# Kernel tuning notes

Measured on AMD Instinct MI355X. Metric: run time of the kernel, lower is better.

The kernel has to match this reference:

```python
import jax, jax.numpy as jnp
import numpy as np

N, C, T, V, K = 32, 256, 64, 25, 3   # batch, in_channels, frames, joints, adjacency partitions
D = 256                               # out_channels
KT = 9                                # temporal kernel size
PAD = (KT - 1) // 2
EPS = 1e-5                            # BatchNorm eps (torch default)


def setup_inputs() -> dict:
    key = jax.random.key(0)
    ks = jax.random.split(key, 5)
    x = jax.random.normal(ks[0], (N, C, T, V), jnp.float32)
    A = jax.random.uniform(ks[1], (K, V, V), jnp.float32)           # learnable adjacency
    W_gcn = jax.random.normal(ks[2], (K, D, C), jnp.float32) * (2.0 / C) ** 0.5  # K stacked 1x1 convs
    b_gcn = jnp.zeros((K, D), jnp.float32)
    W_tcn = jax.random.normal(ks[3], (D, D, KT, 1), jnp.float32) * (2.0 / (D * KT)) ** 0.5  # kaiming fan_out
    b_tcn = jnp.zeros((D,), jnp.float32)
    gamma = jnp.ones((D,), jnp.float32)   # bn_init(bn, 1)
    beta = jnp.zeros((D,), jnp.float32)
    return dict(x=x, A=A, W_gcn=W_gcn, b_gcn=b_gcn, W_tcn=W_tcn,
                b_tcn=b_tcn, gamma=gamma, beta=beta)


def reference(x, A, W_gcn, b_gcn, W_tcn, b_tcn, gamma, beta):
    # ---- GCN: per-partition 1x1 conv over channels, then graph aggregation via A[k], summed over k ----
    # y[k,n,d,t,v] = sum_c W_gcn[k,d,c] * x[n,c,t,v] + b_gcn[k,d]
    y = jnp.einsum('kdc,nctv->kndtv', W_gcn, x) + b_gcn[:, None, :, None, None]
    # aggregate neighbors: sum_v y[k,n,d,t,v] * A[k,v,w], accumulated over partitions k
    y = jnp.einsum('kndtv,kvw->ndtw', y, A)        # [N, D, T, V]

    # ---- TCN: (9,1) temporal conv + BatchNorm2d (batch statistics) ----
    z = jax.lax.conv_general_dilated(
        y, W_tcn, window_strides=(1, 1), padding=((PAD, PAD), (0, 0)),
        dimension_numbers=('NCHW', 'OIHW', 'NCHW'))
    z = z + b_tcn[None, :, None, None]
    mean = jnp.mean(z, axis=(0, 2, 3), keepdims=True)
    var = jnp.mean((z - mean) ** 2, axis=(0, 2, 3), keepdims=True)  # biased, as torch BN training fwd
    z = gamma[None, :, None, None] * (z - mean) * jax.lax.rsqrt(var + EPS) + beta[None, :, None, None]

    # ---- residual (identity branch: in==out, stride==1) + ReLU ----
    return jax.nn.relu(z + x)
```

## Files before the change

### kernel.cpp

```cpp
#include <hip/hip_runtime.h>
#include <math.h>

typedef unsigned short u16;
typedef short v8s __attribute__((ext_vector_type(8)));
typedef float v4f __attribute__((ext_vector_type(4)));

#define AS1 __attribute__((address_space(1)))
#define AS3 __attribute__((address_space(3)))

__device__ __forceinline__ float bf2f(u16 u) {
    union { unsigned int i; float f; } c; c.i = ((unsigned int)u) << 16; return c.f;
}
__device__ __forceinline__ u16 f2bf(float f) {
    union { float f; unsigned int i; } c; c.f = f;
    unsigned int u = c.i;
    return (u16)((u + 0x7FFFu + ((u >> 16) & 1u)) >> 16);
}
__device__ __forceinline__ void gload_lds16(const void* g, void* l) {
    __builtin_amdgcn_global_load_lds((const AS1 void*)(uintptr_t)g,
                                     (AS3 void*)(unsigned int)(uintptr_t)l,
                                     16, 0, 0);
}

#define Nn 32
#define Tt 64
#define Vv 25
#define NP 51200
#define NBLK 200

__global__ __launch_bounds__(256) void prep_kernel(
    const float* __restrict__ Wg, const float* __restrict__ Wt,
    const float* __restrict__ A, const float* __restrict__ bg,
    u16* __restrict__ Wgb, u16* __restrict__ Wtb,
    float* __restrict__ bias2, float* __restrict__ zpad)
{
    const int idx = blockIdx.x * 256 + threadIdx.x;
    const int stride = gridDim.x * 256;
    for (int i = idx; i < 256 * 2304; i += stride) {
        int d = i / 2304, r = i - d * 2304, dt = r >> 8, c = r & 255;
        Wtb[i] = f2bf(Wt[(d * 256 + c) * 9 + dt]);
    }
    for (int i = idx; i < 256 * 768; i += stride) {
        int d = i / 768, r = i - d * 768, k = r >> 8, c = r & 255;
        Wgb[i] = f2bf(Wg[(k * 256 + d) * 256 + c]);
    }
    for (int i = idx; i < 25 * 256; i += stride) {
        int w = i >> 8, d = i & 255;
        float s = 0.f;
        for (int k = 0; k < 3; ++k) {
            float cs = 0.f;
            for (int v = 0; v < 25; ++v) cs += A[(k * 25 + v) * 25 + w];
            s += bg[k * 256 + d] * cs;
        }
        bias2[i] = s;
    }
    for (int i = idx; i < 256; i += stride) zpad[i] = 0.f;
}

__global__ __launch_bounds__(256) void xa_kernel(
    const float* __restrict__ x, const float* __restrict__ A,
    u16* __restrict__ xa2)
{
    const int t = blockIdx.x, n = blockIdx.y;
    const int tid = threadIdx.x;
    __shared__ float xs[256 * 25];

    for (int i = tid; i < 6400; i += 256) {
        int c = i / 25, v = i - c * 25;
        xs[i] = x[((n * 256 + c) * 64 + t) * 25 + v];
    }
    __syncthreads();

    float xr[25];
    #pragma unroll
    for (int v = 0; v < 25; ++v) xr[v] = xs[tid * 25 + v];

    const size_t pbase = ((size_t)n * 64 + t) * 25;
    #pragma unroll 1
    for (int k = 0; k < 3; ++k) {
        float o[25];
        #pragma unroll
        for (int w = 0; w < 25; ++w) {
            float acc = 0.f;
            #pragma unroll
            for (int v = 0; v < 25; ++v)
                acc = fmaf(xr[v], A[(k * 25 + v) * 25 + w], acc);
            o[w] = acc;
        }
        u16* dst = xa2 + k * 256 + tid;
        #pragma unroll
        for (int w = 0; w < 25; ++w)
            dst[(pbase + w) * 768] = f2bf(o[w]);
    }
}

template<int KTOT, bool TCN>
__global__ __launch_bounds__(512) void gemm_kernel(
    const u16* __restrict__ Ad, const u16* __restrict__ Bw,
    const float* __restrict__ bias, u16* __restrict__ outB,
    float* __restrict__ psum, float* __restrict__ psq,
    const u16* __restrict__ zpad)
{
    constexpr int NT = KTOT / 64;
    __shared__ u16 smem[32768];

    const int tid = threadIdx.x;
    const int wid = tid >> 6, lane = tid & 63;
    const int lr = lane & 15, hk = lane >> 4;
    const int wm = wid >> 2, wn = wid & 3;
    const int rA = lane >> 3, sA = lane & 7;

    const int orig = blockIdx.x;
    const int m = (orig & 7) * 25 + (orig >> 3);

    u16* As = smem;
    u16* Bs = smem + 16384;

    v4f acc[8][4];
    const v4f vzero = {0.f, 0.f, 0.f, 0.f};
    #pragma unroll
    for (int mf = 0; mf < 8; ++mf)
        #pragma unroll
        for (int nf = 0; nf < 4; ++nf) acc[mf][nf] = vzero;

    for (int kt = 0; kt < NT; ++kt) {
        #pragma unroll
        for (int i = 0; i < 4; ++i) {
            const int ch = wid + i * 8;
            const int row = ch * 8 + rA;
            const int ss = sA ^ rA;
            const u16* srcA;
            if (TCN) {
                const int dt = kt >> 2, c0 = (kt & 3) << 6;
                const int p = m * 256 + row;
                const int t = (p % 1600) / 25;
                const int tp = t + dt - 4;
                srcA = ((unsigned)tp < 64u)
                     ? (Ad + (size_t)(p + (dt - 4) * 25) * 256 + c0 + ss * 8)
                     : zpad;
            } else {
                srcA = Ad + (size_t)(m * 256 + row) * 768 + kt * 64 + ss * 8;
            }
            gload_lds16(srcA, (char*)As + ch * 1024);
            gload_lds16(Bw + (size_t)row * KTOT + kt * 64 + ss * 8,
                        (char*)Bs + ch * 1024);
        }
        __syncthreads();

        #pragma unroll
        for (int kk = 0; kk < 2; ++kk) {
            v8s a[8], b[4];
            #pragma unroll
            for (int mf = 0; mf < 8; ++mf) {
                const int row = wm * 128 + mf * 16 + lr;
                const int slot = kk * 4 + hk;
                a[mf] = *(const v8s*)((const char*)As + row * 128 + ((slot ^ (row & 7)) << 4));
            }
            #pragma unroll
            for (int nf = 0; nf < 4; ++nf) {
                const int row = wn * 64 + nf * 16 + lr;
                const int slot = kk * 4 + hk;
                b[nf] = *(const v8s*)((const char*)Bs + row * 128 + ((slot ^ (row & 7)) << 4));
            }
            #pragma unroll
            for (int mf = 0; mf < 8; ++mf)
                #pragma unroll
                for (int nf = 0; nf < 4; ++nf)
                    acc[mf][nf] = __builtin_amdgcn_mfma_f32_16x16x32_bf16(
                        a[mf], b[nf], acc[mf][nf], 0, 0, 0);
        }
        __syncthreads();
    }

    if (!TCN) {
        #pragma unroll
        for (int mf = 0; mf < 8; ++mf) {
            #pragma unroll
            for (int j = 0; j < 4; ++j) {
                const int p = m * 256 + wm * 128 + mf * 16 + hk * 4 + j;
                const int w = p % 25;
                #pragma unroll
                for (int nf = 0; nf < 4; ++nf) {
                    const int d = wn * 64 + nf * 16 + lr;
                    outB[(size_t)p * 256 + d] = f2bf(acc[mf][nf][j] + bias[w * 256 + d]);
                }
            }
        }
    } else {
        float s[4], q[4];
        #pragma unroll
        for (int nf = 0; nf < 4; ++nf) {
            const int d = wn * 64 + nf * 16 + lr;
            const float bb = bias[d];
            s[nf] = 0.f; q[nf] = 0.f;
            #pragma unroll
            for (int mf = 0; mf < 8; ++mf) {
                #pragma unroll
                for (int j = 0; j < 4; ++j) {
                    const int p = m * 256 + wm * 128 + mf * 16 + hk * 4 + j;
                    const float zz = acc[mf][nf][j] + bb;
                    outB[(size_t)p * 256 + d] = f2bf(zz);
                    s[nf] += zz; q[nf] += zz * zz;
                }
            }
            s[nf] += __shfl_xor(s[nf], 16); s[nf] += __shfl_xor(s[nf], 32);
            q[nf] += __shfl_xor(q[nf], 16); q[nf] += __shfl_xor(q[nf], 32);
        }
        __syncthreads();
        float* red = (float*)smem;
        if (hk == 0) {
            #pragma unroll
            for (int nf = 0; nf < 4; ++nf) {
                const int d = wn * 64 + nf * 16 + lr;
                red[wm * 256 + d] = s[nf];
                red[512 + wm * 256 + d] = q[nf];
            }
        }
        __syncthreads();
        if (tid < 256) {
            psum[(size_t)tid * NBLK + m] = red[tid] + red[256 + tid];
            psq[(size_t)tid * NBLK + m]  = red[512 + tid] + red[768 + tid];
        }
    }
}

__global__ __launch_bounds__(256) void bn_stats_kernel(
    const float* __restrict__ psum, const float* __restrict__ psq,
    const float* __restrict__ gamma, const float* __restrict__ beta,
    float* __restrict__ scale, float* __restrict__ shift)
{
    const int d = blockIdx.x, tid = threadIdx.x;
    float s = 0.f, q = 0.f;
    for (int i = tid; i < NBLK; i += 256) {
        s += psum[(size_t)d * NBLK + i];
        q += psq[(size_t)d * NBLK + i];
    }
    #pragma unroll
    for (int off = 32; off; off >>= 1) {
        s += __shfl_down(s, off);
        q += __shfl_down(q, off);
    }
    __shared__ float rs[4], rq[4];
    if ((tid & 63) == 0) { rs[tid >> 6] = s; rq[tid >> 6] = q; }
    __syncthreads();
    if (tid == 0) {
        s = rs[0] + rs[1] + rs[2] + rs[3];
        q = rq[0] + rq[1] + rq[2] + rq[3];
        const float mean = s / 51200.f;
        const float var = q / 51200.f - mean * mean;
        const float inv = rsqrtf(var + 1e-5f);
        scale[d] = gamma[d] * inv;
        shift[d] = beta[d] - gamma[d] * inv * mean;
    }
}

__global__ __launch_bounds__(256) void bn_apply_kernel(
    const u16* __restrict__ zb, const float* __restrict__ x,
    const float* __restrict__ scale, const float* __restrict__ shift,
    float* __restrict__ out)
{
    const int chunk = blockIdx.x;
    const int n = blockIdx.y;
    const int tid = threadIdx.x;
    __shared__ u16 zs[128 * 66];
    const size_t p0 = (size_t)n * 1600 + chunk * 64;

    for (int half = 0; half < 2; ++half) {
        const int d0 = half * 128;
        if (half) __syncthreads();
        for (int i = tid; i < 128 * 64; i += 256) {
            const int pl = i >> 7, dl = i & 127;
            zs[dl * 66 + pl] = zb[(p0 + pl) * 256 + d0 + dl];
        }
        __syncthreads();
        for (int i = tid; i < 128 * 64; i += 256) {
            const int dl = i >> 6, j = i & 63;
            const int d = d0 + dl;
            const size_t addr = ((size_t)n * 256 + d) * 1600 + chunk * 64 + j;
            const float r = bf2f(zs[dl * 66 + j]) * scale[d] + shift[d] + x[addr];
            out[addr] = fmaxf(r, 0.f);
        }
    }
}

extern "C" void kernel_launch(void* const* d_in, const int* in_sizes, int n_in,
                              void* d_out, int out_size, void* d_ws, size_t ws_size,
                              hipStream_t stream)
{
    const float* x     = (const float*)d_in[0];
    const float* A     = (const float*)d_in[1];
    const float* Wg    = (const float*)d_in[2];
    const float* bg    = (const float*)d_in[3];
    const float* Wt    = (const float*)d_in[4];
    const float* bt    = (const float*)d_in[5];
    const float* gamma = (const float*)d_in[6];
    const float* beta  = (const float*)d_in[7];
    float* out = (float*)d_out;

    char* w = (char*)d_ws;
    u16*   xa2   = (u16*)(w);
    u16*   y2T   = (u16*)(w + 78643200);
    u16*   zb    = (u16*)(w + 104857600);
    u16*   Wgb   = (u16*)(w + 131072000);
    u16*   Wtb   = (u16*)(w + 131465216);
    float* bias2 = (float*)(w + 132644864);
    float* psum  = (float*)(w + 132670464);
    float* psq   = (float*)(w + 133080064);
    float* scale = (float*)(w + 133489664);
    float* shift = (float*)(w + 133490688);
    float* zpad  = (float*)(w + 133491712);

    prep_kernel<<<128, 256, 0, stream>>>(Wg, Wt, A, bg, Wgb, Wtb, bias2, zpad);
    xa_kernel<<<dim3(64, 32), 256, 0, stream>>>(x, A, xa2);
    gemm_kernel<768, false><<<NBLK, 512, 0, stream>>>(xa2, Wgb, bias2, y2T,
                                                      nullptr, nullptr, (const u16*)zpad);
    gemm_kernel<2304, true><<<NBLK, 512, 0, stream>>>(y2T, Wtb, bt, zb,
                                                      psum, psq, (const u16*)zpad);
    bn_stats_kernel<<<256, 256, 0, stream>>>(psum, psq, gamma, beta, scale, shift);
    bn_apply_kernel<<<dim3(25, 32), 256, 0, stream>>>(zb, x, scale, shift, out);
}
```

Before: 196.8 us.

## Double-buffer LDS tiles with async prefetch two stages ahead in GEMM

Splits the shared-memory tile into two buffers and issues global-to-LDS loads for tile kt+2 while the MFMAs run on the current tile. Explicit vmcnt waits and barriers replace the per-iteration __syncthreads pair. A and B fragments for both k-halves are loaded into registers before the barrier so the buffer can be refilled early, and MFMA priority is raised with s_setprio. The aim is to hide global load latency behind compute, at the cost of twice the LDS (128KB per block), more registers, and a launch_bounds hint of 2 blocks per CU that the LDS size may not allow.

```diff
diff --git a/kernel.cpp b/kernel.cpp
--- a/kernel.cpp
+++ b/kernel.cpp
@@ -95,14 +95,14 @@
 }
 
 template<int KTOT, bool TCN>
-__global__ __launch_bounds__(512) void gemm_kernel(
+__global__ __launch_bounds__(512, 2) void gemm_kernel(
     const u16* __restrict__ Ad, const u16* __restrict__ Bw,
     const float* __restrict__ bias, u16* __restrict__ outB,
     float* __restrict__ psum, float* __restrict__ psq,
     const u16* __restrict__ zpad)
 {
     constexpr int NT = KTOT / 64;
-    __shared__ u16 smem[32768];
+    __shared__ u16 smem[2][32768];
 
     const int tid = threadIdx.x;
     const int wid = tid >> 6, lane = tid & 63;
@@ -113,9 +113,6 @@
     const int orig = blockIdx.x;
     const int m = (orig & 7) * 25 + (orig >> 3);
 
-    u16* As = smem;
-    u16* Bs = smem + 16384;
-
     v4f acc[8][4];
     const v4f vzero = {0.f, 0.f, 0.f, 0.f};
     #pragma unroll
@@ -123,54 +120,103 @@
         #pragma unroll
         for (int nf = 0; nf < 4; ++nf) acc[mf][nf] = vzero;
 
+#define STAGE(buf, ktv)                                                        \
+    {                                                                          \
+        _Pragma("unroll")                                                      \
+        for (int i = 0; i < 4; ++i) {                                          \
+            const int ch = wid + i * 8;                             \
+            const int row = ch * 8 + rA;                           \
+            const int ss = sA ^ rA;                           \
+            const u16* srcA;                                                   \
+            if (TCN) {                                                         \
+                const int dt = (ktv) >> 2, c0 = ((ktv)&3) << 6;                \
+                const int p = m * 256 + row;                                   \
+                const int t = (p % 1600) / 25;                                 \
+                const int tp = t + dt - 4;                                     \
+                srcA = ((unsigned)tp < 64u)                                    \
+                     ? (Ad + (size_t)(p + (dt - 4) * 25) * 256 + c0 + ss * 8)  \
+                     : zpad;                                                   \
+            } else {                                                           \
+                srcA = Ad + (size_t)(m * 256 + row) * 768 + (ktv)*64 + ss * 8; \
+            }                                                                  \
+            gload_lds16(srcA, (char*)&smem[buf][0] + ch * 1024);               \
+            gload_lds16(Bw + (size_t)row * KTOT + (ktv)*64 + ss * 8,           \
+                        (char*)&smem[buf][0] + 32768 + ch * 1024);             \
+        }                                                                      \
+    }
+
+#define LDA_(dst, As_, mfv, kkv)                                               \
+    {                                                                          \
+        const int row = wm * 128 + (mfv)*16 + lr;                              \
+        dst = *(const v8s*)((const char*)(As_) + row * 128 +                   \
+                            ((((kkv)*4 + hk) ^ (row & 7)) << 4));              \
+    }
+#define LDB_(dst, Bs_, nfv, kkv)                                               \
+    {                                                                          \
+        const int row = wn * 64 + (nfv)*16 + lr;                               \
+        dst = *(const v8s*)((const char*)(Bs_) + row * 128 +                   \
+                            ((((kkv)*4 + hk) ^ (row & 7)) << 4));              \
+    }
+
+    STAGE(0, 0);
+    if (NT > 1) STAGE(1, 1);
+    if (NT > 1) asm volatile("s_waitcnt vmcnt(8)" ::: "memory");
+    else        asm volatile("s_waitcnt vmcnt(0)" ::: "memory");
+    __builtin_amdgcn_sched_barrier(0);
+    __builtin_amdgcn_s_barrier();
+
+    #pragma unroll 1
     for (int kt = 0; kt < NT; ++kt) {
-        #pragma unroll
-        for (int i = 0; i < 4; ++i) {
-            const int ch = wid + i * 8;
-            const int row = ch * 8 + rA;
-            const int ss = sA ^ rA;
-            const u16* srcA;
-            if (TCN) {
-                const int dt = kt >> 2, c0 = (kt & 3) << 6;
-                const int p = m * 256 + row;
-                const int t = (p % 1600) / 25;
-                const int tp = t + dt - 4;
-                srcA = ((unsigned)tp < 64u)
-                     ? (Ad + (size_t)(p + (dt - 4) * 25) * 256 + c0 + ss * 8)
-                     : zpad;
-            } else {
-                srcA = Ad + (size_t)(m * 256 + row) * 768 + kt * 64 + ss * 8;
-            }
-            gload_lds16(srcA, (char*)As + ch * 1024);
-            gload_lds16(Bw + (size_t)row * KTOT + kt * 64 + ss * 8,
-                        (char*)Bs + ch * 1024);
-        }
-        __syncthreads();
-
-        #pragma unroll
-        for (int kk = 0; kk < 2; ++kk) {
-            v8s a[8], b[4];
-            #pragma unroll
-            for (int mf = 0; mf < 8; ++mf) {
-                const int row = wm * 128 + mf * 16 + lr;
-                const int slot = kk * 4 + hk;
-                a[mf] = *(const v8s*)((const char*)As + row * 128 + ((slot ^ (row & 7)) << 4));
-            }
-            #pragma unroll
-            for (int nf = 0; nf < 4; ++nf) {
-                const int row = wn * 64 + nf * 16 + lr;
-                const int slot = kk * 4 + hk;
-                b[nf] = *(const v8s*)((const char*)Bs + row * 128 + ((slot ^ (row & 7)) << 4));
-            }
-            #pragma unroll
-            for (int mf = 0; mf < 8; ++mf)
-                #pragma unroll
-                for (int nf = 0; nf < 4; ++nf)
-                    acc[mf][nf] = __builtin_amdgcn_mfma_f32_16x16x32_bf16(
-                        a[mf], b[nf], acc[mf][nf], 0, 0, 0);
-        }
-        __syncthreads();
-    }
+        const int cur = kt & 1;
+        const u16* As = &smem[cur][0];
+        const u16* Bs = As + 16384;
+
+        v8s a0[8], a1[8], b0[4], b1[4];
+        #pragma unroll
+        for (int nf = 0; nf < 4; ++nf) LDB_(b0[nf], Bs, nf, 0);
+        #pragma unroll
+        for (int mf = 0; mf < 8; ++mf) LDA_(a0[mf], As, mf, 0);
+        #pragma unroll
+        for (int nf = 0; nf < 4; ++nf) LDB_(b1[nf], Bs, nf, 1);
+        #pragma unroll
+        for (int mf = 0; mf < 8; ++mf) LDA_(a1[mf], As, mf, 1);
+        asm volatile("s_waitcnt lgkmcnt(0)" ::: "memory");
+        __builtin_amdgcn_sched_barrier(0);
+        __builtin_amdgcn_s_barrier();
+        __builtin_amdgcn_sched_barrier(0);
+
+        if (kt + 2 < NT) STAGE(cur, kt + 2);
+        __builtin_amdgcn_sched_barrier(0);
+
+        __builtin_amdgcn_s_setprio(1);
+        #pragma unroll
+        for (int mf = 0; mf < 8; ++mf)
+            #pragma unroll
+            for (int nf = 0; nf < 4; ++nf)
+                acc[mf][nf] = __builtin_amdgcn_mfma_f32_16x16x32_bf16(
+                    a0[mf], b0[nf], acc[mf][nf], 0, 0, 0);
+        #pragma unroll
+        for (int mf = 0; mf < 8; ++mf)
+            #pragma unroll
+            for (int nf = 0; nf < 4; ++nf)
+                acc[mf][nf] = __builtin_amdgcn_mfma_f32_16x16x32_bf16(
+                    a1[mf], b1[nf], acc[mf][nf], 0, 0, 0);
+        __builtin_amdgcn_s_setprio(0);
+        __builtin_amdgcn_sched_barrier(0);
+
+        if (kt + 2 < NT) {
+            asm volatile("s_waitcnt vmcnt(8)" ::: "memory");
+            __builtin_amdgcn_sched_barrier(0);
+            __builtin_amdgcn_s_barrier();
+        } else if (kt + 1 < NT) {
+            asm volatile("s_waitcnt vmcnt(0)" ::: "memory");
+            __builtin_amdgcn_sched_barrier(0);
+            __builtin_amdgcn_s_barrier();
+        }
+    }
+#undef STAGE
+#undef LDA_
+#undef LDB_
 
     if (!TCN) {
         #pragma unroll
@@ -207,7 +253,7 @@
             q[nf] += __shfl_xor(q[nf], 16); q[nf] += __shfl_xor(q[nf], 32);
         }
         __syncthreads();
-        float* red = (float*)smem;
+        float* red = (float*)&smem[0][0];
         if (hk == 0) {
             #pragma unroll
             for (int nf = 0; nf < 4; ++nf) {
```

After: 186.3 us. 1.06x faster.

## Pre-pack weights into MFMA fragment order and halve GEMM M-tile

Applied to the files above, without the earlier changes.

The prep kernel now writes both weight matrices in the exact per-lane MFMA fragment order. Each wave then loads its B operands straight from global memory into registers, so B no longer goes through LDS. The M tile per block shrinks from 256 to 128 rows and the grid grows from 200 to 400 blocks, which fills more CUs and cuts LDS and register use. The trade-off is that B fragments are re-read from cache by every block and wave with no LDS sharing, and each block now does less reuse per load.

```diff
diff --git a/kernel.cpp b/kernel.cpp
--- a/kernel.cpp
+++ b/kernel.cpp
@@ -26,23 +26,31 @@
 #define Tt 64
 #define Vv 25
 #define NP 51200
-#define NBLK 200
+#define NBLK 400
 
 __global__ __launch_bounds__(256) void prep_kernel(
     const float* __restrict__ Wg, const float* __restrict__ Wt,
     const float* __restrict__ A, const float* __restrict__ bg,
-    u16* __restrict__ Wgb, u16* __restrict__ Wtb,
+    u16* __restrict__ Bpg, u16* __restrict__ Bpt,
     float* __restrict__ bias2, float* __restrict__ zpad)
 {
     const int idx = blockIdx.x * 256 + threadIdx.x;
     const int stride = gridDim.x * 256;
-    for (int i = idx; i < 256 * 2304; i += stride) {
-        int d = i / 2304, r = i - d * 2304, dt = r >> 8, c = r & 255;
-        Wtb[i] = f2bf(Wt[(d * 256 + c) * 9 + dt]);
-    }
-    for (int i = idx; i < 256 * 768; i += stride) {
-        int d = i / 768, r = i - d * 768, k = r >> 8, c = r & 255;
-        Wgb[i] = f2bf(Wg[(k * 256 + d) * 256 + c]);
+    for (int i = idx; i < 589824; i += stride) {
+        const int e = i & 7, lane = (i >> 3) & 63, rest = i >> 9;
+        const int kk = rest & 1, nf = (rest >> 1) & 3, wn = (rest >> 3) & 3, kt = rest >> 5;
+        const int d = wn * 64 + nf * 16 + (lane & 15);
+        const int k = kt * 64 + kk * 32 + (lane >> 4) * 8 + e;
+        const int dt = k >> 8, c = k & 255;
+        Bpt[i] = f2bf(Wt[(d * 256 + c) * 9 + dt]);
+    }
+    for (int i = idx; i < 196608; i += stride) {
+        const int e = i & 7, lane = (i >> 3) & 63, rest = i >> 9;
+        const int kk = rest & 1, nf = (rest >> 1) & 3, wn = (rest >> 3) & 3, kt = rest >> 5;
+        const int d = wn * 64 + nf * 16 + (lane & 15);
+        const int k = kt * 64 + kk * 32 + (lane >> 4) * 8 + e;
+        const int k3 = k >> 8, c = k & 255;
+        Bpg[i] = f2bf(Wg[(k3 * 256 + d) * 256 + c]);
     }
     for (int i = idx; i < 25 * 256; i += stride) {
         int w = i >> 8, d = i & 255;
@@ -96,13 +104,13 @@
 
 template<int KTOT, bool TCN>
 __global__ __launch_bounds__(512) void gemm_kernel(
-    const u16* __restrict__ Ad, const u16* __restrict__ Bw,
+    const u16* __restrict__ Ad, const u16* __restrict__ Bp,
     const float* __restrict__ bias, u16* __restrict__ outB,
     float* __restrict__ psum, float* __restrict__ psq,
     const u16* __restrict__ zpad)
 {
     constexpr int NT = KTOT / 64;
-    __shared__ u16 smem[32768];
+    __shared__ u16 smem[8192];
 
     const int tid = threadIdx.x;
     const int wid = tid >> 6, lane = tid & 63;
@@ -111,73 +119,74 @@
     const int rA = lane >> 3, sA = lane & 7;
 
     const int orig = blockIdx.x;
-    const int m = (orig & 7) * 25 + (orig >> 3);
+    const int m = (orig & 7) * 50 + (orig >> 3);
 
     u16* As = smem;
-    u16* Bs = smem + 16384;
-
-    v4f acc[8][4];
+
+    v4f acc[4][4];
     const v4f vzero = {0.f, 0.f, 0.f, 0.f};
     #pragma unroll
-    for (int mf = 0; mf < 8; ++mf)
+    for (int mf = 0; mf < 4; ++mf)
         #pragma unroll
         for (int nf = 0; nf < 4; ++nf) acc[mf][nf] = vzero;
 
     for (int kt = 0; kt < NT; ++kt) {
-        #pragma unroll
-        for (int i = 0; i < 4; ++i) {
+        v8s b[4][2];
+        {
+            const u16* bw = Bp + (((size_t)kt * 4 + wn) << 12) + lane * 8;
+            #pragma unroll
+            for (int nf = 0; nf < 4; ++nf)
+                #pragma unroll
+                for (int kk = 0; kk < 2; ++kk)
+                    b[nf][kk] = *(const v8s*)(bw + ((nf * 2 + kk) << 9));
+        }
+        #pragma unroll
+        for (int i = 0; i < 2; ++i) {
             const int ch = wid + i * 8;
             const int row = ch * 8 + rA;
             const int ss = sA ^ rA;
             const u16* srcA;
             if (TCN) {
                 const int dt = kt >> 2, c0 = (kt & 3) << 6;
-                const int p = m * 256 + row;
+                const int p = m * 128 + row;
                 const int t = (p % 1600) / 25;
                 const int tp = t + dt - 4;
                 srcA = ((unsigned)tp < 64u)
                      ? (Ad + (size_t)(p + (dt - 4) * 25) * 256 + c0 + ss * 8)
                      : zpad;
             } else {
-                srcA = Ad + (size_t)(m * 256 + row) * 768 + kt * 64 + ss * 8;
+                srcA = Ad + (size_t)(m * 128 + row) * 768 + kt * 64 + ss * 8;
             }
             gload_lds16(srcA, (char*)As + ch * 1024);
-            gload_lds16(Bw + (size_t)row * KTOT + kt * 64 + ss * 8,
-                        (char*)Bs + ch * 1024);
-        }
-        __syncthreads();
-
-        #pragma unroll
-        for (int kk = 0; kk < 2; ++kk) {
-            v8s a[8], b[4];
-            #pragma unroll
-            for (int mf = 0; mf < 8; ++mf) {
-                const int row = wm * 128 + mf * 16 + lr;
+        }
+        __syncthreads();
+
+        v8s a[4][2];
+        #pragma unroll
+        for (int mf = 0; mf < 4; ++mf)
+            #pragma unroll
+            for (int kk = 0; kk < 2; ++kk) {
+                const int row = wm * 64 + mf * 16 + lr;
                 const int slot = kk * 4 + hk;
-                a[mf] = *(const v8s*)((const char*)As + row * 128 + ((slot ^ (row & 7)) << 4));
-            }
-            #pragma unroll
-            for (int nf = 0; nf < 4; ++nf) {
-                const int row = wn * 64 + nf * 16 + lr;
-                const int slot = kk * 4 + hk;
-                b[nf] = *(const v8s*)((const char*)Bs + row * 128 + ((slot ^ (row & 7)) << 4));
-            }
-            #pragma unroll
-            for (int mf = 0; mf < 8; ++mf)
+                a[mf][kk] = *(const v8s*)((const char*)As + row * 128 + ((slot ^ (row & 7)) << 4));
+            }
+        #pragma unroll
+        for (int kk = 0; kk < 2; ++kk)
+            #pragma unroll
+            for (int mf = 0; mf < 4; ++mf)
                 #pragma unroll
                 for (int nf = 0; nf < 4; ++nf)
                     acc[mf][nf] = __builtin_amdgcn_mfma_f32_16x16x32_bf16(
-                        a[mf], b[nf], acc[mf][nf], 0, 0, 0);
-        }
+                        a[mf][kk], b[nf][kk], acc[mf][nf], 0, 0, 0);
         __syncthreads();
     }
 
     if (!TCN) {
         #pragma unroll
-        for (int mf = 0; mf < 8; ++mf) {
+        for (int mf = 0; mf < 4; ++mf) {
             #pragma unroll
             for (int j = 0; j < 4; ++j) {
-                const int p = m * 256 + wm * 128 + mf * 16 + hk * 4 + j;
+                const int p = m * 128 + wm * 64 + mf * 16 + hk * 4 + j;
                 const int w = p % 25;
                 #pragma unroll
                 for (int nf = 0; nf < 4; ++nf) {
@@ -194,10 +203,10 @@
             const float bb = bias[d];
             s[nf] = 0.f; q[nf] = 0.f;
             #pragma unroll
-            for (int mf = 0; mf < 8; ++mf) {
+            for (int mf = 0; mf < 4; ++mf) {
                 #pragma unroll
                 for (int j = 0; j < 4; ++j) {
-                    const int p = m * 256 + wm * 128 + mf * 16 + hk * 4 + j;
+                    const int p = m * 128 + wm * 64 + mf * 16 + hk * 4 + j;
                     const float zz = acc[mf][nf][j] + bb;
                     outB[(size_t)p * 256 + d] = f2bf(zz);
                     s[nf] += zz; q[nf] += zz * zz;
@@ -301,8 +310,8 @@
     u16*   xa2   = (u16*)(w);
     u16*   y2T   = (u16*)(w + 78643200);
     u16*   zb    = (u16*)(w + 104857600);
-    u16*   Wgb   = (u16*)(w + 131072000);
-    u16*   Wtb   = (u16*)(w + 131465216);
+    u16*   Bpg   = (u16*)(w + 131072000);
+    u16*   Bpt   = (u16*)(w + 131465216);
     float* bias2 = (float*)(w + 132644864);
     float* psum  = (float*)(w + 132670464);
     float* psq   = (float*)(w + 133080064);
@@ -310,11 +319,11 @@
     float* shift = (float*)(w + 133490688);
     float* zpad  = (float*)(w + 133491712);
 
-    prep_kernel<<<128, 256, 0, stream>>>(Wg, Wt, A, bg, Wgb, Wtb, bias2, zpad);
+    prep_kernel<<<256, 256, 0, stream>>>(Wg, Wt, A, bg, Bpg, Bpt, bias2, zpad);
     xa_kernel<<<dim3(64, 32), 256, 0, stream>>>(x, A, xa2);
-    gemm_kernel<768, false><<<NBLK, 512, 0, stream>>>(xa2, Wgb, bias2, y2T,
+    gemm_kernel<768, false><<<NBLK, 512, 0, stream>>>(xa2, Bpg, bias2, y2T,
                                                       nullptr, nullptr, (const u16*)zpad);
-    gemm_kernel<2304, true><<<NBLK, 512, 0, stream>>>(y2T, Wtb, bt, zb,
+    gemm_kernel<2304, true><<<NBLK, 512, 0, stream>>>(y2T, Bpt, bt, zb,
                                                       psum, psq, (const u16*)zpad);
     bn_stats_kernel<<<256, 256, 0, stream>>>(psum, psq, gamma, beta, scale, shift);
     bn_apply_kernel<<<dim3(25, 32), 256, 0, stream>>>(zb, x, scale, shift, out);
```

Result: slower. 221.1 us (+12.3%).
